# Kernel optimization log

Measured on AMD Instinct MI355X. Metric: run time of the kernel, lower is better.

## Reference

```python
import jax, jax.numpy as jnp
import numpy as np
import math

HIDDEN = 1024
HEADS = 16
HEADDIM = HIDDEN // HEADS
K_PROJ = 256
MAX_POS = 4096
BSZ, QLEN = 4, 4096


def setup_inputs() -> dict:
    key = jax.random.key(0)
    ks = jax.random.split(key, 7)
    hiddenstates = jax.random.normal(ks[0], (BSZ, QLEN, HIDDEN), dtype=jnp.float32)
    # torch nn.Linear weights: [out_features, in_features], applied as x @ W.T
    Wq = jax.random.normal(ks[1], (HIDDEN, HIDDEN), dtype=jnp.float32) * 0.02
    Wk = jax.random.normal(ks[2], (HIDDEN, HIDDEN), dtype=jnp.float32) * 0.02
    Wv = jax.random.normal(ks[3], (HIDDEN, HIDDEN), dtype=jnp.float32) * 0.02
    Wo = jax.random.normal(ks[4], (HIDDEN, HIDDEN), dtype=jnp.float32) * 0.02
    # Linformer low-rank projections (scaled for numerical sanity)
    E = jax.random.normal(ks[5], (MAX_POS, K_PROJ), dtype=jnp.float32) / math.sqrt(MAX_POS)
    F = jax.random.normal(ks[6], (MAX_POS, K_PROJ), dtype=jnp.float32) / math.sqrt(MAX_POS)
    return {"hiddenstates": hiddenstates, "Wq": Wq, "Wk": Wk, "Wv": Wv, "Wo": Wo, "E": E, "F": F}


def reference(hiddenstates, Wq, Wk, Wv, Wo, E, F):
    bsz, qlen, _ = hiddenstates.shape
    # projections (torch Linear: x @ W.T)
    q = hiddenstates @ Wq.T  # [b, s, h*d]
    k = hiddenstates @ Wk.T
    v = hiddenstates @ Wv.T
    # [b, heads, s, d]
    q = q.reshape(bsz, qlen, HEADS, HEADDIM).transpose(0, 2, 1, 3)
    k = k.reshape(bsz, qlen, HEADS, HEADDIM).transpose(0, 2, 1, 3)
    v = v.reshape(bsz, qlen, HEADS, HEADDIM).transpose(0, 2, 1, 3)
    if qlen > K_PROJ:
        Et = E[:qlen, :]  # [s, k]
        Ft = F[:qlen, :]
        # compress K/V along sequence: [b, heads, k, d]
        k = jnp.einsum('sk,bhsd->bhkd', Et, k)
        v = jnp.einsum('sk,bhsd->bhkd', Ft, v)
    scores = jnp.einsum('bhqd,bhkd->bhqk', q, k) / math.sqrt(HEADDIM)
    attn = jax.nn.softmax(scores.astype(jnp.float32), axis=-1).astype(q.dtype)
    out = jnp.einsum('bhqk,bhkd->bhqd', attn, v)  # [b, heads, s, d]
    out = out.transpose(0, 2, 1, 3).reshape(bsz, qlen, HIDDEN)
    return out @ Wo.T
```

## Files before the change

kernel.cpp:

```cpp
#include <hip/hip_runtime.h>

typedef unsigned short u16;
typedef unsigned int u32;
typedef __attribute__((ext_vector_type(8))) __bf16 bf16x8;
typedef __attribute__((ext_vector_type(4))) float f32x4;
typedef __attribute__((ext_vector_type(8))) u16 u16x8;
typedef __attribute__((ext_vector_type(4))) u16 u16x4;

typedef const __attribute__((address_space(1))) u32* gas_p;
typedef __attribute__((address_space(3))) u32* las_p;

__device__ __forceinline__ void gload16(const void* g, void* l) {
  __builtin_amdgcn_global_load_lds((gas_p)g, (las_p)l, 16, 0, 0);
}

__device__ __forceinline__ u16 f2bf(float f) {
  u32 u = __builtin_bit_cast(u32, f);
  u32 r = (u + 0x7fffu + ((u >> 16) & 1u)) >> 16;
  return (u16)r;
}

__global__ __launch_bounds__(256) void conv_hs(const float* __restrict__ in,
                                               u16* __restrict__ out_row,
                                               u16* __restrict__ out_t) {
  __shared__ u16 t[32][34];
  const int r0 = blockIdx.x * 32, c0 = blockIdx.y * 32;
  const int lx = threadIdx.x & 31, ly = threadIdx.x >> 5;
#pragma unroll
  for (int i = 0; i < 4; ++i) {
    const int r = r0 + ly + i * 8;
    const u16 v = f2bf(in[(size_t)r * 1024 + c0 + lx]);
    out_row[(size_t)r * 1024 + c0 + lx] = v;
    t[ly + i * 8][lx] = v;
  }
  __syncthreads();
  const int b = r0 >> 12, s0 = r0 & 4095;
#pragma unroll
  for (int i = 0; i < 4; ++i)
    out_t[((size_t)b * 1024 + c0 + ly + i * 8) * 4096 + s0 + lx] = t[lx][ly + i * 8];
}

__global__ __launch_bounds__(256) void conv_w4(const float* __restrict__ a,
                                               const float* __restrict__ b,
                                               const float* __restrict__ c,
                                               const float* __restrict__ d,
                                               u16* __restrict__ out) {
  const float* src = blockIdx.y == 0 ? a : blockIdx.y == 1 ? b : blockIdx.y == 2 ? c : d;
  const int i = (blockIdx.x * 256 + threadIdx.x) * 4;
  const float4 v = *(const float4*)(src + i);
  u16x4 o = {f2bf(v.x), f2bf(v.y), f2bf(v.z), f2bf(v.w)};
  *(u16x4*)(out + (size_t)blockIdx.y * 1048576 + i) = o;
}

__global__ __launch_bounds__(256) void transpose_conv(const float* __restrict__ in,
                                                      u16* __restrict__ out) {
  const int R = 4096, Cc = 256;
  __shared__ float t[32][33];
  const int r0 = blockIdx.x * 32, c0 = blockIdx.y * 32;
  const int lx = threadIdx.x & 31, ly = threadIdx.x >> 5;
#pragma unroll
  for (int i = 0; i < 4; ++i)
    t[ly + i * 8][lx] = in[(size_t)(r0 + ly + i * 8) * Cc + c0 + lx];
  __syncthreads();
#pragma unroll
  for (int i = 0; i < 4; ++i)
    out[(size_t)(c0 + ly + i * 8) * R + r0 + lx] = f2bf(t[lx][ly + i * 8]);
}

template <int OUTBF>
__global__ __launch_bounds__(256) void gemm_bt(const u16* __restrict__ A,
                                               const u16* __restrict__ B,
                                               void* __restrict__ C, int M, int N,
                                               int K) {
  __shared__ u16 lds[2][128 * 64];
  const int tid = threadIdx.x, l = tid & 63, w = tid >> 6;
  const int m0 = blockIdx.x * 128, n0 = blockIdx.y * 128;
  const int wr = w >> 1, wc = w & 1;
  f32x4 acc[4][4] = {};
  for (int k0 = 0; k0 < K; k0 += 64) {
#pragma unroll
    for (int i = 0; i < 4; ++i) {
      const int c = i * 256 + tid;
      const int row = c >> 3;
      const int scb = ((c & 7) << 4) ^ ((row & 7) << 4);
      gload16((const char*)A + ((size_t)(m0 + row) * K + k0) * 2 + scb,
              (char*)&lds[0][0] + (size_t)(i * 256 + w * 64) * 16);
      gload16((const char*)B + ((size_t)(n0 + row) * K + k0) * 2 + scb,
              (char*)&lds[1][0] + (size_t)(i * 256 + w * 64) * 16);
    }
    __syncthreads();
#pragma unroll
    for (int kk = 0; kk < 2; ++kk) {
      bf16x8 af[4], bf[4];
#pragma unroll
      for (int f = 0; f < 4; ++f) {
        const int ra = wr * 64 + f * 16 + (l & 15);
        af[f] = *(const bf16x8*)((const char*)&lds[0][0] + ra * 128 +
                                 (((l >> 4) * 16 + kk * 64) ^ ((ra & 7) << 4)));
        const int rb = wc * 64 + f * 16 + (l & 15);
        bf[f] = *(const bf16x8*)((const char*)&lds[1][0] + rb * 128 +
                                 (((l >> 4) * 16 + kk * 64) ^ ((rb & 7) << 4)));
      }
#pragma unroll
      for (int mf = 0; mf < 4; ++mf)
#pragma unroll
        for (int nf = 0; nf < 4; ++nf)
          acc[mf][nf] = __builtin_amdgcn_mfma_f32_16x16x32_bf16(af[mf], bf[nf],
                                                                acc[mf][nf], 0, 0, 0);
    }
    __syncthreads();
  }
#pragma unroll
  for (int mf = 0; mf < 4; ++mf) {
    const int rbase = m0 + wr * 64 + mf * 16 + ((l >> 4) << 2);
#pragma unroll
    for (int nf = 0; nf < 4; ++nf) {
      const int cc = n0 + wc * 64 + nf * 16 + (l & 15);
#pragma unroll
      for (int j = 0; j < 4; ++j) {
        if (OUTBF)
          ((u16*)C)[(size_t)(rbase + j) * N + cc] = f2bf(acc[mf][nf][j]);
        else
          ((float*)C)[(size_t)(rbase + j) * N + cc] = acc[mf][nf][j];
      }
    }
  }
}

__global__ __launch_bounds__(256) void proj64(const u16* __restrict__ EFt,
                                              const u16* __restrict__ hsT2,
                                              u16* __restrict__ hsEF) {
  __shared__ u16 lA[64 * 64], lB[128 * 64];
  const int tid = threadIdx.x, l = tid & 63, w = tid >> 6;
  const int m0 = blockIdx.x * 64, n0 = blockIdx.y * 128, b = blockIdx.z;
  const u16* Bp = hsT2 + (size_t)b * 1024 * 4096;
  const int wr = w >> 1, wc = w & 1;
  f32x4 acc[2][4] = {};
  for (int k0 = 0; k0 < 4096; k0 += 64) {
#pragma unroll
    for (int i = 0; i < 2; ++i) {
      const int c = i * 256 + tid;
      const int row = c >> 3;
      const int scb = ((c & 7) << 4) ^ ((row & 7) << 4);
      gload16((const char*)EFt + ((size_t)(m0 + row) * 4096 + k0) * 2 + scb,
              (char*)lA + (size_t)(i * 256 + w * 64) * 16);
    }
#pragma unroll
    for (int i = 0; i < 4; ++i) {
      const int c = i * 256 + tid;
      const int row = c >> 3;
      const int scb = ((c & 7) << 4) ^ ((row & 7) << 4);
      gload16((const char*)Bp + ((size_t)(n0 + row) * 4096 + k0) * 2 + scb,
              (char*)lB + (size_t)(i * 256 + w * 64) * 16);
    }
    __syncthreads();
#pragma unroll
    for (int kk = 0; kk < 2; ++kk) {
      bf16x8 af[2], bf[4];
#pragma unroll
      for (int f = 0; f < 2; ++f) {
        const int ra = wr * 32 + f * 16 + (l & 15);
        af[f] = *(const bf16x8*)((const char*)lA + ra * 128 +
                                 (((l >> 4) * 16 + kk * 64) ^ ((ra & 7) << 4)));
      }
#pragma unroll
      for (int f = 0; f < 4; ++f) {
        const int rb = wc * 64 + f * 16 + (l & 15);
        bf[f] = *(const bf16x8*)((const char*)lB + rb * 128 +
                                 (((l >> 4) * 16 + kk * 64) ^ ((rb & 7) << 4)));
      }
#pragma unroll
      for (int mf = 0; mf < 2; ++mf)
#pragma unroll
        for (int nf = 0; nf < 4; ++nf)
          acc[mf][nf] = __builtin_amdgcn_mfma_f32_16x16x32_bf16(af[mf], bf[nf],
                                                                acc[mf][nf], 0, 0, 0);
    }
    __syncthreads();
  }
#pragma unroll
  for (int mf = 0; mf < 2; ++mf) {
    const int rbase = m0 + wr * 32 + mf * 16 + ((l >> 4) << 2);
#pragma unroll
    for (int nf = 0; nf < 4; ++nf) {
      const int cc = n0 + wc * 64 + nf * 16 + (l & 15);
#pragma unroll
      for (int j = 0; j < 4; ++j)
        hsEF[((size_t)b * 512 + rbase + j) * 1024 + cc] = f2bf(acc[mf][nf][j]);
    }
  }
}

__global__ __launch_bounds__(256) void gemm_kv(const u16* __restrict__ hsEF,
                                               const u16* __restrict__ Wk,
                                               const u16* __restrict__ Wv,
                                               u16* __restrict__ kproj,
                                               u16* __restrict__ vprojT) {
  __shared__ u16 lA[64 * 64], lB[128 * 64];
  const int tid = threadIdx.x, l = tid & 63, w = tid >> 6;
  const int m0 = blockIdx.x * 64, n0 = blockIdx.y * 128;
  const int b = m0 >> 9, half = (m0 >> 8) & 1;
  const u16* Bp = half ? Wv : Wk;
  const int wr = w >> 1, wc = w & 1;
  f32x4 acc[2][4] = {};
  for (int k0 = 0; k0 < 1024; k0 += 64) {
#pragma unroll
    for (int i = 0; i < 2; ++i) {
      const int c = i * 256 + tid;
      const int row = c >> 3;
      const int scb = ((c & 7) << 4) ^ ((row & 7) << 4);
      gload16((const char*)hsEF + ((size_t)(m0 + row) * 1024 + k0) * 2 + scb,
              (char*)lA + (size_t)(i * 256 + w * 64) * 16);
    }
#pragma unroll
    for (int i = 0; i < 4; ++i) {
      const int c = i * 256 + tid;
      const int row = c >> 3;
      const int scb = ((c & 7) << 4) ^ ((row & 7) << 4);
      gload16((const char*)Bp + ((size_t)(n0 + row) * 1024 + k0) * 2 + scb,
              (char*)lB + (size_t)(i * 256 + w * 64) * 16);
    }
    __syncthreads();
#pragma unroll
    for (int kk = 0; kk < 2; ++kk) {
      bf16x8 af[2], bf[4];
#pragma unroll
      for (int f = 0; f < 2; ++f) {
        const int ra = wr * 32 + f * 16 + (l & 15);
        af[f] = *(const bf16x8*)((const char*)lA + ra * 128 +
                                 (((l >> 4) * 16 + kk * 64) ^ ((ra & 7) << 4)));
      }
#pragma unroll
      for (int f = 0; f < 4; ++f) {
        const int rb = wc * 64 + f * 16 + (l & 15);
        bf[f] = *(const bf16x8*)((const char*)lB + rb * 128 +
                                 (((l >> 4) * 16 + kk * 64) ^ ((rb & 7) << 4)));
      }
#pragma unroll
      for (int mf = 0; mf < 2; ++mf)
#pragma unroll
        for (int nf = 0; nf < 4; ++nf)
          acc[mf][nf] = __builtin_amdgcn_mfma_f32_16x16x32_bf16(af[mf], bf[nf],
                                                                acc[mf][nf], 0, 0, 0);
    }
    __syncthreads();
  }
#pragma unroll
  for (int mf = 0; mf < 2; ++mf) {
    const int kp0 = (m0 & 255) + wr * 32 + mf * 16 + ((l >> 4) << 2);
#pragma unroll
    for (int nf = 0; nf < 4; ++nf) {
      const int n = n0 + wc * 64 + nf * 16 + (l & 15);
      if (!half) {
#pragma unroll
        for (int j = 0; j < 4; ++j)
          kproj[((size_t)b * 256 + kp0 + j) * 1024 + n] = f2bf(acc[mf][nf][j]);
      } else {
        u16x4 o = {f2bf(acc[mf][nf][0]), f2bf(acc[mf][nf][1]), f2bf(acc[mf][nf][2]),
                   f2bf(acc[mf][nf][3])};
        *(u16x4*)(vprojT + ((size_t)b * 1024 + n) * 256 + kp0) = o;
      }
    }
  }
}

__global__ __launch_bounds__(256) void attn_kernel(const u16* __restrict__ qmat,
                                                   const u16* __restrict__ kproj,
                                                   const u16* __restrict__ vprojT,
                                                   u16* __restrict__ aout) {
  __shared__ u16 smem[32768];
  const int tid = threadIdx.x, l = tid & 63, w = tid >> 6;
  const int qt = blockIdx.x, h = blockIdx.y, b = blockIdx.z;
  const int qbase = qt * 64;

#pragma unroll
  for (int i = 0; i < 8; ++i) {
    const int c = i * 256 + tid;
    const int row = c >> 3;
    const int scb = ((c & 7) << 4) ^ ((row & 7) << 4);
    gload16((const char*)kproj + (((size_t)(b * 256 + row)) * 1024 + h * 64) * 2 + scb,
            (char*)smem + (size_t)(i * 256 + w * 64) * 16);
  }
#pragma unroll
  for (int i = 0; i < 8; ++i) {
    const int c = i * 256 + tid;
    const int d = c >> 5;
    const int scb = ((c & 31) << 4) ^ ((d & 31) << 4);
    gload16((const char*)vprojT + ((size_t)(b * 1024 + h * 64 + d)) * 256 * 2 + scb,
            (char*)smem + 32768 + (size_t)(i * 256 + w * 64) * 16);
  }
  __syncthreads();

  const u16* qrow =
      qmat + ((size_t)(b * 4096 + qbase + w * 16 + (l & 15))) * 1024 + h * 64;
  bf16x8 qa[2];
#pragma unroll
  for (int kf = 0; kf < 2; ++kf)
    qa[kf] = *(const bf16x8*)(qrow + kf * 32 + (l >> 4) * 8);

  f32x4 s[16] = {};
#pragma unroll
  for (int nf = 0; nf < 16; ++nf) {
    const int kr = nf * 16 + (l & 15);
#pragma unroll
    for (int kf = 0; kf < 2; ++kf) {
      const bf16x8 kb = *(const bf16x8*)((const char*)smem + kr * 128 +
                                         ((kf * 64 + (l >> 4) * 16) ^ ((kr & 7) << 4)));
      s[nf] = __builtin_amdgcn_mfma_f32_16x16x32_bf16(qa[kf], kb, s[nf], 0, 0, 0);
    }
  }

  float mx[4] = {-1e30f, -1e30f, -1e30f, -1e30f}, sum[4] = {0.f, 0.f, 0.f, 0.f};
#pragma unroll
  for (int j = 0; j < 4; ++j) {
#pragma unroll
    for (int nf = 0; nf < 16; ++nf) mx[j] = fmaxf(mx[j], s[nf][j]);
#pragma unroll
    for (int m = 1; m < 16; m <<= 1) mx[j] = fmaxf(mx[j], __shfl_xor(mx[j], m, 64));
  }
#pragma unroll
  for (int nf = 0; nf < 16; ++nf)
#pragma unroll
    for (int j = 0; j < 4; ++j) {
      const float e = __expf((s[nf][j] - mx[j]) * 0.125f);
      s[nf][j] = e;
      sum[j] += e;
    }
#pragma unroll
  for (int j = 0; j < 4; ++j) {
#pragma unroll
    for (int m = 1; m < 16; m <<= 1) sum[j] += __shfl_xor(sum[j], m, 64);
    sum[j] = 1.0f / sum[j];
  }

  __syncthreads();

  u16* Pw = smem + w * 4096;
#pragma unroll
  for (int nf = 0; nf < 16; ++nf) {
    const int col = nf * 16 + (l & 15);
#pragma unroll
    for (int j = 0; j < 4; ++j) {
      const int row = (l >> 4) * 4 + j;
      *(u16*)((char*)Pw + row * 512 + ((col * 2) ^ (row << 4))) =
          f2bf(s[nf][j] * sum[j]);
    }
  }
  __syncthreads();

  f32x4 o[4] = {};
#pragma unroll
  for (int kf = 0; kf < 8; ++kf) {
    const int q = l & 15;
    const bf16x8 pb = *(const bf16x8*)((const char*)Pw + q * 512 +
                                       ((kf * 64 + (l >> 4) * 16) ^ (q << 4)));
#pragma unroll
    for (int mf = 0; mf < 4; ++mf) {
      const int d = mf * 16 + (l & 15);
      const bf16x8 va = *(const bf16x8*)((const char*)smem + 32768 + d * 512 +
                                         ((kf * 64 + (l >> 4) * 16) ^ ((d & 31) << 4)));
      o[mf] = __builtin_amdgcn_mfma_f32_16x16x32_bf16(va, pb, o[mf], 0, 0, 0);
    }
  }

#pragma unroll
  for (int mf = 0; mf < 4; ++mf) {
    const int d0 = mf * 16 + ((l >> 4) << 2);
    const int srow = b * 4096 + qbase + w * 16 + (l & 15);
    u16x4 ov = {f2bf(o[mf][0]), f2bf(o[mf][1]), f2bf(o[mf][2]), f2bf(o[mf][3])};
    *(u16x4*)(aout + (size_t)srow * 1024 + h * 64 + d0) = ov;
  }
}

extern "C" void kernel_launch(void* const* d_in, const int* in_sizes, int n_in,
                              void* d_out, int out_size, void* d_ws, size_t ws_size,
                              hipStream_t stream) {
  const float* hs = (const float*)d_in[0];
  const float* Wq = (const float*)d_in[1];
  const float* Wk = (const float*)d_in[2];
  const float* Wv = (const float*)d_in[3];
  const float* Wo = (const float*)d_in[4];
  const float* E = (const float*)d_in[5];
  const float* F = (const float*)d_in[6];

  char* ws = (char*)d_ws;
  u16* hs_bf = (u16*)(ws + 0);
  u16* hsT2 = (u16*)(ws + 33554432);
  u16* aout = hsT2;
  u16* qout = (u16*)(ws + 67108864);
  u16* Wall = (u16*)(ws + 100663296);
  u16* EFt = (u16*)(ws + 109051904);
  u16* hsEF = (u16*)(ws + 113246208);
  u16* kproj = (u16*)(ws + 117440512);
  u16* vprojT = (u16*)(ws + 119537664);

  conv_hs<<<dim3(512, 32), 256, 0, stream>>>(hs, hs_bf, hsT2);
  conv_w4<<<dim3(1024, 4), 256, 0, stream>>>(Wq, Wk, Wv, Wo, Wall);
  transpose_conv<<<dim3(128, 8), 256, 0, stream>>>(E, EFt);
  transpose_conv<<<dim3(128, 8), 256, 0, stream>>>(F, EFt + (size_t)256 * 4096);

  gemm_bt<1><<<dim3(128, 8), 256, 0, stream>>>(hs_bf, Wall, qout, 16384, 1024, 1024);
  proj64<<<dim3(8, 8, 4), 256, 0, stream>>>(EFt, hsT2, hsEF);
  gemm_kv<<<dim3(32, 8), 256, 0, stream>>>(hsEF, Wall + 1048576, Wall + 2097152,
                                           kproj, vprojT);
  attn_kernel<<<dim3(64, 16, 4), 256, 0, stream>>>(qout, kproj, vprojT, aout);
  gemm_bt<0><<<dim3(128, 8), 256, 0, stream>>>(aout, Wall + 3145728, d_out, 16384,
                                               1024, 1024);
}
```

Measured before the change: 369.5 us.

## Read K/V directly from global in attention, defer softmax normalization

The attention kernel no longer stages the compressed K and transposed V tiles into shared memory. The MFMA operands are loaded straight from global memory, which relies on L2/L1 reuse across the 64 query tiles that share a (b,h). The 1/sum normalization moves from the P write to the output store, using shuffles to line up row sums with the output lane layout. One __syncthreads is dropped, and LDS shrinks to 32KB, which allows higher occupancy. The trade is more global load traffic and latency exposed inside the MFMA loops.

```diff
diff --git a/kernel.cpp b/kernel.cpp
--- a/kernel.cpp
+++ b/kernel.cpp
@@ -268,29 +268,11 @@
                                                    const u16* __restrict__ kproj,
                                                    const u16* __restrict__ vprojT,
                                                    u16* __restrict__ aout) {
-  __shared__ u16 smem[32768];
+  __shared__ u16 smem[16384];
   const int tid = threadIdx.x, l = tid & 63, w = tid >> 6;
   const int qt = blockIdx.x, h = blockIdx.y, b = blockIdx.z;
   const int qbase = qt * 64;
 
-#pragma unroll
-  for (int i = 0; i < 8; ++i) {
-    const int c = i * 256 + tid;
-    const int row = c >> 3;
-    const int scb = ((c & 7) << 4) ^ ((row & 7) << 4);
-    gload16((const char*)kproj + (((size_t)(b * 256 + row)) * 1024 + h * 64) * 2 + scb,
-            (char*)smem + (size_t)(i * 256 + w * 64) * 16);
-  }
-#pragma unroll
-  for (int i = 0; i < 8; ++i) {
-    const int c = i * 256 + tid;
-    const int d = c >> 5;
-    const int scb = ((c & 31) << 4) ^ ((d & 31) << 4);
-    gload16((const char*)vprojT + ((size_t)(b * 1024 + h * 64 + d)) * 256 * 2 + scb,
-            (char*)smem + 32768 + (size_t)(i * 256 + w * 64) * 16);
-  }
-  __syncthreads();
-
   const u16* qrow =
       qmat + ((size_t)(b * 4096 + qbase + w * 16 + (l & 15))) * 1024 + h * 64;
   bf16x8 qa[2];
@@ -298,14 +280,15 @@
   for (int kf = 0; kf < 2; ++kf)
     qa[kf] = *(const bf16x8*)(qrow + kf * 32 + (l >> 4) * 8);
 
+  const u16* kbase = kproj + ((size_t)(b * 256)) * 1024 + h * 64;
   f32x4 s[16] = {};
 #pragma unroll
   for (int nf = 0; nf < 16; ++nf) {
     const int kr = nf * 16 + (l & 15);
 #pragma unroll
     for (int kf = 0; kf < 2; ++kf) {
-      const bf16x8 kb = *(const bf16x8*)((const char*)smem + kr * 128 +
-                                         ((kf * 64 + (l >> 4) * 16) ^ ((kr & 7) << 4)));
+      const bf16x8 kb =
+          *(const bf16x8*)(kbase + (size_t)kr * 1024 + kf * 32 + (l >> 4) * 8);
       s[nf] = __builtin_amdgcn_mfma_f32_16x16x32_bf16(qa[kf], kb, s[nf], 0, 0, 0);
     }
   }
@@ -327,13 +310,17 @@
       sum[j] += e;
     }
 #pragma unroll
-  for (int j = 0; j < 4; ++j) {
+  for (int j = 0; j < 4; ++j)
 #pragma unroll
     for (int m = 1; m < 16; m <<= 1) sum[j] += __shfl_xor(sum[j], m, 64);
-    sum[j] = 1.0f / sum[j];
-  }
-
-  __syncthreads();
+
+  float bs0 = __shfl(sum[0], ((l & 15) >> 2) << 4, 64);
+  float bs1 = __shfl(sum[1], ((l & 15) >> 2) << 4, 64);
+  float bs2 = __shfl(sum[2], ((l & 15) >> 2) << 4, 64);
+  float bs3 = __shfl(sum[3], ((l & 15) >> 2) << 4, 64);
+  const float r01 = (l & 1) ? bs1 : bs0;
+  const float r23 = (l & 1) ? bs3 : bs2;
+  const float rs = 1.0f / ((l & 2) ? r23 : r01);
 
   u16* Pw = smem + w * 4096;
 #pragma unroll
@@ -342,12 +329,12 @@
 #pragma unroll
     for (int j = 0; j < 4; ++j) {
       const int row = (l >> 4) * 4 + j;
-      *(u16*)((char*)Pw + row * 512 + ((col * 2) ^ (row << 4))) =
-          f2bf(s[nf][j] * sum[j]);
+      *(u16*)((char*)Pw + row * 512 + ((col * 2) ^ (row << 4))) = f2bf(s[nf][j]);
     }
   }
   __syncthreads();
 
+  const u16* vbase = vprojT + ((size_t)(b * 1024 + h * 64)) * 256;
   f32x4 o[4] = {};
 #pragma unroll
   for (int kf = 0; kf < 8; ++kf) {
@@ -357,8 +344,8 @@
 #pragma unroll
     for (int mf = 0; mf < 4; ++mf) {
       const int d = mf * 16 + (l & 15);
-      const bf16x8 va = *(const bf16x8*)((const char*)smem + 32768 + d * 512 +
-                                         ((kf * 64 + (l >> 4) * 16) ^ ((d & 31) << 4)));
+      const bf16x8 va =
+          *(const bf16x8*)(vbase + (size_t)d * 256 + kf * 32 + (l >> 4) * 8);
       o[mf] = __builtin_amdgcn_mfma_f32_16x16x32_bf16(va, pb, o[mf], 0, 0, 0);
     }
   }
@@ -367,7 +354,8 @@
   for (int mf = 0; mf < 4; ++mf) {
     const int d0 = mf * 16 + ((l >> 4) << 2);
     const int srow = b * 4096 + qbase + w * 16 + (l & 15);
-    u16x4 ov = {f2bf(o[mf][0]), f2bf(o[mf][1]), f2bf(o[mf][2]), f2bf(o[mf][3])};
+    u16x4 ov = {f2bf(o[mf][0] * rs), f2bf(o[mf][1] * rs), f2bf(o[mf][2] * rs),
+                f2bf(o[mf][3] * rs)};
     *(u16x4*)(aout + (size_t)srow * 1024 + h * 64 + d0) = ov;
   }
 }
```

New measurement: 447.4 us. 1.21x slower.

## Process two query tiles per attention block to reuse staged K/V

Applied to the files above, without the earlier changes.

Each attention block now handles 128 queries instead of 64, so the K and V tiles loaded into shared memory are reused across two query tiles and the grid is halved. Softmax normalization is deferred: unnormalized probabilities are written as bf16 and the output is scaled by the reciprocal row sum, which is redistributed across lanes with shuffles. Register pressure roughly doubles for the score accumulators, which may lower occupancy, and the P buffer is reused between the two tiles.

```diff
diff --git a/kernel.cpp b/kernel.cpp
--- a/kernel.cpp
+++ b/kernel.cpp
@@ -271,7 +271,7 @@
   __shared__ u16 smem[32768];
   const int tid = threadIdx.x, l = tid & 63, w = tid >> 6;
   const int qt = blockIdx.x, h = blockIdx.y, b = blockIdx.z;
-  const int qbase = qt * 64;
+  const int qbase = qt * 128;
 
 #pragma unroll
   for (int i = 0; i < 8; ++i) {
@@ -291,14 +291,17 @@
   }
   __syncthreads();
 
-  const u16* qrow =
-      qmat + ((size_t)(b * 4096 + qbase + w * 16 + (l & 15))) * 1024 + h * 64;
-  bf16x8 qa[2];
-#pragma unroll
-  for (int kf = 0; kf < 2; ++kf)
-    qa[kf] = *(const bf16x8*)(qrow + kf * 32 + (l >> 4) * 8);
-
-  f32x4 s[16] = {};
+  bf16x8 qa[2][2];
+#pragma unroll
+  for (int t = 0; t < 2; ++t) {
+    const u16* qrow =
+        qmat + ((size_t)(b * 4096 + qbase + t * 64 + w * 16 + (l & 15))) * 1024 + h * 64;
+#pragma unroll
+    for (int kf = 0; kf < 2; ++kf)
+      qa[t][kf] = *(const bf16x8*)(qrow + kf * 32 + (l >> 4) * 8);
+  }
+
+  f32x4 s0[16] = {}, s1[16] = {};
 #pragma unroll
   for (int nf = 0; nf < 16; ++nf) {
     const int kr = nf * 16 + (l & 15);
@@ -306,69 +309,142 @@
     for (int kf = 0; kf < 2; ++kf) {
       const bf16x8 kb = *(const bf16x8*)((const char*)smem + kr * 128 +
                                          ((kf * 64 + (l >> 4) * 16) ^ ((kr & 7) << 4)));
-      s[nf] = __builtin_amdgcn_mfma_f32_16x16x32_bf16(qa[kf], kb, s[nf], 0, 0, 0);
-    }
-  }
-
-  float mx[4] = {-1e30f, -1e30f, -1e30f, -1e30f}, sum[4] = {0.f, 0.f, 0.f, 0.f};
-#pragma unroll
-  for (int j = 0; j < 4; ++j) {
-#pragma unroll
-    for (int nf = 0; nf < 16; ++nf) mx[j] = fmaxf(mx[j], s[nf][j]);
-#pragma unroll
-    for (int m = 1; m < 16; m <<= 1) mx[j] = fmaxf(mx[j], __shfl_xor(mx[j], m, 64));
-  }
-#pragma unroll
-  for (int nf = 0; nf < 16; ++nf)
+      s0[nf] = __builtin_amdgcn_mfma_f32_16x16x32_bf16(qa[0][kf], kb, s0[nf], 0, 0, 0);
+      s1[nf] = __builtin_amdgcn_mfma_f32_16x16x32_bf16(qa[1][kf], kb, s1[nf], 0, 0, 0);
+    }
+  }
+
+  float rs0, rs1;
+  {
+    float mx[4] = {-1e30f, -1e30f, -1e30f, -1e30f}, sum[4] = {0.f, 0.f, 0.f, 0.f};
 #pragma unroll
     for (int j = 0; j < 4; ++j) {
-      const float e = __expf((s[nf][j] - mx[j]) * 0.125f);
-      s[nf][j] = e;
-      sum[j] += e;
-    }
-#pragma unroll
-  for (int j = 0; j < 4; ++j) {
-#pragma unroll
-    for (int m = 1; m < 16; m <<= 1) sum[j] += __shfl_xor(sum[j], m, 64);
-    sum[j] = 1.0f / sum[j];
+#pragma unroll
+      for (int nf = 0; nf < 16; ++nf) mx[j] = fmaxf(mx[j], s0[nf][j]);
+#pragma unroll
+      for (int m = 1; m < 16; m <<= 1) mx[j] = fmaxf(mx[j], __shfl_xor(mx[j], m, 64));
+    }
+#pragma unroll
+    for (int nf = 0; nf < 16; ++nf)
+#pragma unroll
+      for (int j = 0; j < 4; ++j) {
+        const float e = __expf((s0[nf][j] - mx[j]) * 0.125f);
+        s0[nf][j] = e;
+        sum[j] += e;
+      }
+#pragma unroll
+    for (int j = 0; j < 4; ++j)
+#pragma unroll
+      for (int m = 1; m < 16; m <<= 1) sum[j] += __shfl_xor(sum[j], m, 64);
+    const float bs0 = __shfl(sum[0], ((l & 15) >> 2) << 4, 64);
+    const float bs1 = __shfl(sum[1], ((l & 15) >> 2) << 4, 64);
+    const float bs2 = __shfl(sum[2], ((l & 15) >> 2) << 4, 64);
+    const float bs3 = __shfl(sum[3], ((l & 15) >> 2) << 4, 64);
+    const float r01 = (l & 1) ? bs1 : bs0;
+    const float r23 = (l & 1) ? bs3 : bs2;
+    rs0 = 1.0f / ((l & 2) ? r23 : r01);
+  }
+  {
+    float mx[4] = {-1e30f, -1e30f, -1e30f, -1e30f}, sum[4] = {0.f, 0.f, 0.f, 0.f};
+#pragma unroll
+    for (int j = 0; j < 4; ++j) {
+#pragma unroll
+      for (int nf = 0; nf < 16; ++nf) mx[j] = fmaxf(mx[j], s1[nf][j]);
+#pragma unroll
+      for (int m = 1; m < 16; m <<= 1) mx[j] = fmaxf(mx[j], __shfl_xor(mx[j], m, 64));
+    }
+#pragma unroll
+    for (int nf = 0; nf < 16; ++nf)
+#pragma unroll
+      for (int j = 0; j < 4; ++j) {
+        const float e = __expf((s1[nf][j] - mx[j]) * 0.125f);
+        s1[nf][j] = e;
+        sum[j] += e;
+      }
+#pragma unroll
+    for (int j = 0; j < 4; ++j)
+#pragma unroll
+      for (int m = 1; m < 16; m <<= 1) sum[j] += __shfl_xor(sum[j], m, 64);
+    const float bs0 = __shfl(sum[0], ((l & 15) >> 2) << 4, 64);
+    const float bs1 = __shfl(sum[1], ((l & 15) >> 2) << 4, 64);
+    const float bs2 = __shfl(sum[2], ((l & 15) >> 2) << 4, 64);
+    const float bs3 = __shfl(sum[3], ((l & 15) >> 2) << 4, 64);
+    const float r01 = (l & 1) ? bs1 : bs0;
+    const float r23 = (l & 1) ? bs3 : bs2;
+    rs1 = 1.0f / ((l & 2) ? r23 : r01);
   }
 
   __syncthreads();
 
   u16* Pw = smem + w * 4096;
+  const u16* vb = (const u16*)((const char*)smem + 32768);
+
 #pragma unroll
   for (int nf = 0; nf < 16; ++nf) {
     const int col = nf * 16 + (l & 15);
 #pragma unroll
     for (int j = 0; j < 4; ++j) {
       const int row = (l >> 4) * 4 + j;
-      *(u16*)((char*)Pw + row * 512 + ((col * 2) ^ (row << 4))) =
-          f2bf(s[nf][j] * sum[j]);
-    }
-  }
-  __syncthreads();
-
-  f32x4 o[4] = {};
-#pragma unroll
-  for (int kf = 0; kf < 8; ++kf) {
-    const int q = l & 15;
-    const bf16x8 pb = *(const bf16x8*)((const char*)Pw + q * 512 +
-                                       ((kf * 64 + (l >> 4) * 16) ^ (q << 4)));
+      *(u16*)((char*)Pw + row * 512 + ((col * 2) ^ (row << 4))) = f2bf(s0[nf][j]);
+    }
+  }
+  {
+    f32x4 o[4] = {};
+#pragma unroll
+    for (int kf = 0; kf < 8; ++kf) {
+      const int q = l & 15;
+      const bf16x8 pb = *(const bf16x8*)((const char*)Pw + q * 512 +
+                                         ((kf * 64 + (l >> 4) * 16) ^ (q << 4)));
+#pragma unroll
+      for (int mf = 0; mf < 4; ++mf) {
+        const int d = mf * 16 + (l & 15);
+        const bf16x8 va = *(const bf16x8*)((const char*)vb + d * 512 +
+                                           ((kf * 64 + (l >> 4) * 16) ^ ((d & 31) << 4)));
+        o[mf] = __builtin_amdgcn_mfma_f32_16x16x32_bf16(va, pb, o[mf], 0, 0, 0);
+      }
+    }
 #pragma unroll
     for (int mf = 0; mf < 4; ++mf) {
-      const int d = mf * 16 + (l & 15);
-      const bf16x8 va = *(const bf16x8*)((const char*)smem + 32768 + d * 512 +
-                                         ((kf * 64 + (l >> 4) * 16) ^ ((d & 31) << 4)));
-      o[mf] = __builtin_amdgcn_mfma_f32_16x16x32_bf16(va, pb, o[mf], 0, 0, 0);
-    }
-  }
-
-#pragma unroll
-  for (int mf = 0; mf < 4; ++mf) {
-    const int d0 = mf * 16 + ((l >> 4) << 2);
-    const int srow = b * 4096 + qbase + w * 16 + (l & 15);
-    u16x4 ov = {f2bf(o[mf][0]), f2bf(o[mf][1]), f2bf(o[mf][2]), f2bf(o[mf][3])};
-    *(u16x4*)(aout + (size_t)srow * 1024 + h * 64 + d0) = ov;
+      const int d0 = mf * 16 + ((l >> 4) << 2);
+      const int srow = b * 4096 + qbase + w * 16 + (l & 15);
+      u16x4 ov = {f2bf(o[mf][0] * rs0), f2bf(o[mf][1] * rs0), f2bf(o[mf][2] * rs0),
+                  f2bf(o[mf][3] * rs0)};
+      *(u16x4*)(aout + (size_t)srow * 1024 + h * 64 + d0) = ov;
+    }
+  }
+
+#pragma unroll
+  for (int nf = 0; nf < 16; ++nf) {
+    const int col = nf * 16 + (l & 15);
+#pragma unroll
+    for (int j = 0; j < 4; ++j) {
+      const int row = (l >> 4) * 4 + j;
+      *(u16*)((char*)Pw + row * 512 + ((col * 2) ^ (row << 4))) = f2bf(s1[nf][j]);
+    }
+  }
+  {
+    f32x4 o[4] = {};
+#pragma unroll
+    for (int kf = 0; kf < 8; ++kf) {
+      const int q = l & 15;
+      const bf16x8 pb = *(const bf16x8*)((const char*)Pw + q * 512 +
+                                         ((kf * 64 + (l >> 4) * 16) ^ (q << 4)));
+#pragma unroll
+      for (int mf = 0; mf < 4; ++mf) {
+        const int d = mf * 16 + (l & 15);
+        const bf16x8 va = *(const bf16x8*)((const char*)vb + d * 512 +
+                                           ((kf * 64 + (l >> 4) * 16) ^ ((d & 31) << 4)));
+        o[mf] = __builtin_amdgcn_mfma_f32_16x16x32_bf16(va, pb, o[mf], 0, 0, 0);
+      }
+    }
+#pragma unroll
+    for (int mf = 0; mf < 4; ++mf) {
+      const int d0 = mf * 16 + ((l >> 4) << 2);
+      const int srow = b * 4096 + qbase + 64 + w * 16 + (l & 15);
+      u16x4 ov = {f2bf(o[mf][0] * rs1), f2bf(o[mf][1] * rs1), f2bf(o[mf][2] * rs1),
+                  f2bf(o[mf][3] * rs1)};
+      *(u16x4*)(aout + (size_t)srow * 1024 + h * 64 + d0) = ov;
+    }
   }
 }
 
@@ -403,7 +479,7 @@
   proj64<<<dim3(8, 8, 4), 256, 0, stream>>>(EFt, hsT2, hsEF);
   gemm_kv<<<dim3(32, 8), 256, 0, stream>>>(hsEF, Wall + 1048576, Wall + 2097152,
                                            kproj, vprojT);
-  attn_kernel<<<dim3(64, 16, 4), 256, 0, stream>>>(qout, kproj, vprojT, aout);
+  attn_kernel<<<dim3(32, 16, 4), 256, 0, stream>>>(qout, kproj, vprojT, aout);
   gemm_bt<0><<<dim3(128, 8), 256, 0, stream>>>(aout, Wall + 3145728, d_out, 16384,
                                                1024, 1024);
 }
```

Result: slower. 380.8 us (+3.1%).
